# Performance work log

Measured on AMD Instinct MI355X. Metric: run time of the kernel, lower is better.

The kernel has to match this reference:

```python
import jax, jax.numpy as jnp
import numpy as np

U, I, D, L, NNZ, B = 100000, 50000, 64, 3, 3200000, 4096
N = U + I
MOMENTUM = 0.05

def setup_inputs() -> dict:
    key = jax.random.key(0)
    ks = jax.random.split(key, 10)
    return {
        'user_emb': jax.random.normal(ks[0], (U, D), jnp.float32) * 0.02,
        'item_emb': jax.random.normal(ks[1], (I, D), jnp.float32) * 0.02,
        'W': jax.random.normal(ks[2], (D, D), jnp.float32) * (1.0 / np.sqrt(D)),
        'b': jnp.zeros((D,), jnp.float32),
        'adj_rows': jax.random.randint(ks[3], (NNZ,), 0, N, jnp.int32),
        'adj_cols': jax.random.randint(ks[4], (NNZ,), 0, N, jnp.int32),
        'adj_vals': jax.random.uniform(ks[5], (NNZ,), jnp.float32) * 0.05,
        'users': jax.random.randint(ks[6], (B,), 0, U, jnp.int32),
        'items': jax.random.randint(ks[7], (B,), 0, I, jnp.int32),
        'u_his': jax.random.normal(ks[8], (U, D), jnp.float32),
        'i_his': jax.random.normal(ks[9], (I, D), jnp.float32),
    }

def _spmm(rows, cols, vals, x):
    # y = A @ x for sparse COO A: gather source rows, scale, scatter-add to dest rows
    return jax.ops.segment_sum(vals[:, None] * x[cols], rows, num_segments=N)

def reference(user_emb, item_emb, W, b, adj_rows, adj_cols, adj_vals, users, items, u_his, i_his):
    ego = jnp.concatenate([user_emb, item_emb], axis=0)  # [N, D]
    acc = ego
    cur = ego
    for _ in range(L):
        cur = _spmm(adj_rows, adj_cols, adj_vals, cur)
        acc = acc + cur
    all_emb = acc / (L + 1)           # mean over stacked layers
    u_all = all_emb[:U]
    i_all = all_emb[U:]
    u_online = u_all[users]           # [B, D]
    i_online = i_all[items]
    m = MOMENTUM
    u_target = jax.lax.stop_gradient(u_his[users] * m + u_online * (1.0 - m))
    i_target = jax.lax.stop_gradient(i_his[items] * m + i_online * (1.0 - m))
    p_u = u_online @ W.T + b
    p_i = i_online @ W.T + b
    return (p_u, u_target, p_i, i_target)
```

## Files before the change

### kernel.cpp

```cpp
#include <hip/hip_runtime.h>
#include <hip/hip_bf16.h>

#define U_CNT   100000
#define I_CNT   50000
#define D_DIM   64
#define N_NODES 150000
#define NNZ_E   3200000
#define B_SZ    4096

#define NSUB 1172
#define CAP2 4096
#define TILE_E 8192
#define N_TILES ((NNZ_E + TILE_E - 1) / TILE_E)

#define CONV_THREADS (N_NODES * 16)
#define CONV_PER_BLK (512 * 4)
#define CONV_BLOCKS ((CONV_THREADS + CONV_PER_BLK - 1) / CONV_PER_BLK)

typedef unsigned int uint;
typedef unsigned short ushort_t;
typedef _Float16 half_t;
typedef half_t half2_t __attribute__((ext_vector_type(2)));

union h2u_t { uint u; half2_t h; };
__device__ __forceinline__ half2_t u2h2(uint u) { h2u_t c; c.u = u; return c.h; }
__device__ __forceinline__ uint h22u(half2_t h) { h2u_t c; c.h = h; return c.u; }
__device__ __forceinline__ half2_t h2shfl_xor(half2_t v, int m) {
    h2u_t c; c.h = v; c.u = (uint)__shfl_xor((int)c.u, m, 64); return c.h;
}
__device__ __forceinline__ float h2lo(uint u) { return (float)u2h2(u)[0]; }
__device__ __forceinline__ float h2hi(uint u) { return (float)u2h2(u)[1]; }

__global__ __launch_bounds__(512) void scatter_kernel(const int* __restrict__ rows,
                                                      const int* __restrict__ cols,
                                                      const float* __restrict__ vals,
                                                      int* __restrict__ subcursor,
                                                      int2* __restrict__ meta,
                                                      const float4* __restrict__ ue4,
                                                      const float4* __restrict__ ie4,
                                                      uint2* __restrict__ e2) {
    int tid = threadIdx.x;

    if (blockIdx.x >= N_TILES) {
        int g0 = (blockIdx.x - N_TILES) * CONV_PER_BLK + tid;
        #pragma unroll
        for (int k = 0; k < 4; ++k) {
            int g = g0 + k * 512;
            if (g < CONV_THREADS) {
                float4 f = (g < U_CNT * 16) ? ue4[g] : ie4[g - U_CNT * 16];
                half2_t a = { (half_t)f.x, (half_t)f.y };
                half2_t b = { (half_t)f.z, (half_t)f.w };
                uint2 o; o.x = h22u(a); o.y = h22u(b);
                e2[g] = o;
            }
        }
        return;
    }

    __shared__ int lcnt[NSUB];
    __shared__ int gbase[NSUB];

    for (int i = tid; i < NSUB; i += 512) lcnt[i] = 0;
    __syncthreads();

    int base = blockIdx.x * TILE_E;
    int nk = NNZ_E - base - tid;
    nk = (nk <= 0) ? 0 : (nk + 511) >> 9;

    int pk[16]; float vv[16]; int sb[16]; int rk[16];
    #pragma unroll
    for (int k = 0; k < 16; ++k) {
        if (k < nk) {
            int j = base + tid + (k << 9);
            int r = rows[j];
            int c = cols[j];
            vv[k] = vals[j];
            sb[k] = r >> 7;
            pk[k] = ((r & 127) << 18) | c;
            rk[k] = atomicAdd(&lcnt[sb[k]], 1);
        }
    }
    __syncthreads();

    for (int i = tid; i < NSUB; i += 512) {
        int c = lcnt[i];
        int off = (c > 0) ? atomicAdd(&subcursor[i], c) : 0;
        gbase[i] = i * CAP2 + off;
    }
    __syncthreads();

    #pragma unroll
    for (int k = 0; k < 16; ++k) {
        if (k < nk) {
            int pos = gbase[sb[k]] + rk[k];
            if (pos < (sb[k] + 1) * CAP2)
                meta[pos] = make_int2(pk[k], __float_as_int(vv[k]));
        }
    }
}

__global__ __launch_bounds__(512) void sort_spmm_kernel(const int* __restrict__ subcursor,
                                                        int2* __restrict__ meta,
                                                        int* __restrict__ rstart,
                                                        int* __restrict__ rend,
                                                        const ushort_t* __restrict__ x,
                                                        ushort_t* __restrict__ out) {
    __shared__ int2 stage[CAP2];
    __shared__ int rcnt[128];
    __shared__ int rs[128];
    __shared__ int re_[128];
    int g = blockIdx.x;
    int base = g * CAP2;
    int cnt = subcursor[g];
    if (cnt > CAP2) cnt = CAP2;
    int tid = threadIdx.x;
    int r0 = g << 7;

    if (tid < 128) rcnt[tid] = 0;
    __syncthreads();

    int2 ek[8]; int rk[8];
    int nk = cnt - tid;
    nk = (nk <= 0) ? 0 : (nk + 511) >> 9;
    #pragma unroll
    for (int k = 0; k < 8; ++k) {
        if (k < nk) {
            ek[k] = meta[base + tid + (k << 9)];
            rk[k] = atomicAdd(&rcnt[((uint)ek[k].x >> 18) & 127], 1);
        }
    }
    __syncthreads();

    if (tid < 64) {
        int c0 = rcnt[2 * tid], c1 = rcnt[2 * tid + 1];
        int s2 = c0 + c1, incl = s2;
        #pragma unroll
        for (int off = 1; off < 64; off <<= 1) {
            int t = __shfl_up(incl, off, 64);
            if (tid >= off) incl += t;
        }
        int s0 = incl - s2, s1 = incl - c1;
        rs[2 * tid] = s0;      re_[2 * tid] = s0 + c0;
        rs[2 * tid + 1] = s1;  re_[2 * tid + 1] = incl;
        int r = r0 + 2 * tid;
        if (r < N_NODES)     { rstart[r]     = base + s0; rend[r]     = base + s0 + c0; }
        if (r + 1 < N_NODES) { rstart[r + 1] = base + s1; rend[r + 1] = base + incl;    }
    }
    __syncthreads();

    #pragma unroll
    for (int k = 0; k < 8; ++k) {
        if (k < nk) {
            int rl = ((uint)ek[k].x >> 18) & 127;
            int pos = rs[rl] + rk[k];
            float v = __int_as_float(ek[k].y);
            half2_t hv = { (half_t)v, (half_t)v };
            int2 f = make_int2(ek[k].x & 0x3FFFF, (int)h22u(hv));
            stage[pos] = f;
            meta[base + pos] = f;
        }
    }
    __syncthreads();

    int wv   = tid >> 6;
    int lane = tid & 63;
    int sub  = lane >> 3;
    int l8   = lane & 7;
    const uint4* x4 = (const uint4*)x;

    for (int rr = 0; rr < 16; ++rr) {
        int rl = (wv << 4) + rr;
        int s = rs[rl], e = re_[rl];
        half2_t a0 = { (half_t)0, (half_t)0 };
        half2_t a1 = a0, a2 = a0, a3 = a0;

        if (e > s) {
            int last = e - 1;
            auto ldl = [&](int jj) -> int2 {
                int2 c = stage[jj < e ? jj : last];
                if (jj >= e) c.y = 0;
                return c;
            };
            int j = s + sub;
            int2 c0 = ldl(j);
            int2 c1 = ldl(j + 8);
            int2 c2 = ldl(j + 16);
            int2 c3 = ldl(j + 24);
            for (; j < e; j += 32) {
                uint4 x0 = x4[(size_t)(c0.x & 0x3FFFF) * 8 + l8];
                uint4 x1 = x4[(size_t)(c1.x & 0x3FFFF) * 8 + l8];
                uint4 x2 = x4[(size_t)(c2.x & 0x3FFFF) * 8 + l8];
                uint4 x3 = x4[(size_t)(c3.x & 0x3FFFF) * 8 + l8];
                int jn = j + 32;
                int2 n0 = ldl(jn);
                int2 n1 = ldl(jn + 8);
                int2 n2 = ldl(jn + 16);
                int2 n3 = ldl(jn + 24);
                half2_t v0 = u2h2((uint)c0.y);
                a0 += u2h2(x0.x) * v0; a1 += u2h2(x0.y) * v0;
                a2 += u2h2(x0.z) * v0; a3 += u2h2(x0.w) * v0;
                half2_t v1 = u2h2((uint)c1.y);
                a0 += u2h2(x1.x) * v1; a1 += u2h2(x1.y) * v1;
                a2 += u2h2(x1.z) * v1; a3 += u2h2(x1.w) * v1;
                half2_t v2 = u2h2((uint)c2.y);
                a0 += u2h2(x2.x) * v2; a1 += u2h2(x2.y) * v2;
                a2 += u2h2(x2.z) * v2; a3 += u2h2(x2.w) * v2;
                half2_t v3 = u2h2((uint)c3.y);
                a0 += u2h2(x3.x) * v3; a1 += u2h2(x3.y) * v3;
                a2 += u2h2(x3.z) * v3; a3 += u2h2(x3.w) * v3;
                c0 = n0; c1 = n1; c2 = n2; c3 = n3;
            }
        }
        a0 += h2shfl_xor(a0, 8);  a1 += h2shfl_xor(a1, 8);
        a2 += h2shfl_xor(a2, 8);  a3 += h2shfl_xor(a3, 8);
        a0 += h2shfl_xor(a0, 16); a1 += h2shfl_xor(a1, 16);
        a2 += h2shfl_xor(a2, 16); a3 += h2shfl_xor(a3, 16);
        a0 += h2shfl_xor(a0, 32); a1 += h2shfl_xor(a1, 32);
        a2 += h2shfl_xor(a2, 32); a3 += h2shfl_xor(a3, 32);

        int wid = r0 + rl;
        if (sub == 0 && wid < N_NODES) {
            uint4 r;
            r.x = h22u(a0); r.y = h22u(a1); r.z = h22u(a2); r.w = h22u(a3);
            ((uint4*)out)[(size_t)wid * 8 + l8] = r;
        }
    }
}

__global__ __launch_bounds__(256) void spmm_fp16_kernel(const int* __restrict__ rstart,
                                                        const int* __restrict__ rend,
                                                        const int2* __restrict__ csr,
                                                        const ushort_t* __restrict__ x,
                                                        ushort_t* __restrict__ out) {
    int wid  = (blockIdx.x * blockDim.x + threadIdx.x) >> 6;
    int lane = threadIdx.x & 63;
    int sub  = lane >> 3;
    int l8   = lane & 7;
    if (wid >= N_NODES) return;
    int s = rstart[wid], e = rend[wid];
    const uint4* x4 = (const uint4*)x;

    int last = e - 1; if (last < s) last = s;
    auto ld = [&](int jj) -> int2 {
        int2 c = csr[jj < e ? jj : last];
        if (jj >= e) c.y = 0;
        return c;
    };

    half2_t a0 = { (half_t)0, (half_t)0 };
    half2_t a1 = a0, a2 = a0, a3 = a0;

    int j = s + sub;
    int2 c0 = ld(j);
    int2 c1 = ld(j + 8);
    int2 c2 = ld(j + 16);
    int2 c3 = ld(j + 24);
    for (; j < e; j += 32) {
        uint4 x0 = x4[(size_t)(c0.x & 0x3FFFF) * 8 + l8];
        uint4 x1 = x4[(size_t)(c1.x & 0x3FFFF) * 8 + l8];
        uint4 x2 = x4[(size_t)(c2.x & 0x3FFFF) * 8 + l8];
        uint4 x3 = x4[(size_t)(c3.x & 0x3FFFF) * 8 + l8];
        int jn = j + 32;
        int2 n0 = ld(jn);
        int2 n1 = ld(jn + 8);
        int2 n2 = ld(jn + 16);
        int2 n3 = ld(jn + 24);
        half2_t v0 = u2h2((uint)c0.y);
        a0 += u2h2(x0.x) * v0; a1 += u2h2(x0.y) * v0;
        a2 += u2h2(x0.z) * v0; a3 += u2h2(x0.w) * v0;
        half2_t v1 = u2h2((uint)c1.y);
        a0 += u2h2(x1.x) * v1; a1 += u2h2(x1.y) * v1;
        a2 += u2h2(x1.z) * v1; a3 += u2h2(x1.w) * v1;
        half2_t v2 = u2h2((uint)c2.y);
        a0 += u2h2(x2.x) * v2; a1 += u2h2(x2.y) * v2;
        a2 += u2h2(x2.z) * v2; a3 += u2h2(x2.w) * v2;
        half2_t v3 = u2h2((uint)c3.y);
        a0 += u2h2(x3.x) * v3; a1 += u2h2(x3.y) * v3;
        a2 += u2h2(x3.z) * v3; a3 += u2h2(x3.w) * v3;
        c0 = n0; c1 = n1; c2 = n2; c3 = n3;
    }
    a0 += h2shfl_xor(a0, 8);  a1 += h2shfl_xor(a1, 8);
    a2 += h2shfl_xor(a2, 8);  a3 += h2shfl_xor(a3, 8);
    a0 += h2shfl_xor(a0, 16); a1 += h2shfl_xor(a1, 16);
    a2 += h2shfl_xor(a2, 16); a3 += h2shfl_xor(a3, 16);
    a0 += h2shfl_xor(a0, 32); a1 += h2shfl_xor(a1, 32);
    a2 += h2shfl_xor(a2, 32); a3 += h2shfl_xor(a3, 32);

    if (sub == 0) {
        uint4 r;
        r.x = h22u(a0); r.y = h22u(a1); r.z = h22u(a2); r.w = h22u(a3);
        ((uint4*)out)[(size_t)wid * 8 + l8] = r;
    }
}

__global__ __launch_bounds__(256) void epilogue_kernel(const int* __restrict__ users,
                                                       const int* __restrict__ items,
                                                       const int* __restrict__ rstart,
                                                       const int* __restrict__ rend,
                                                       const int2* __restrict__ csr,
                                                       const ushort_t* __restrict__ ebuf,
                                                       const ushort_t* __restrict__ buf1,
                                                       const ushort_t* __restrict__ buf2,
                                                       const float* __restrict__ u_his,
                                                       const float* __restrict__ i_his,
                                                       const float* __restrict__ W,
                                                       const float* __restrict__ bvec,
                                                       float* __restrict__ out) {
    __shared__ float Wt[D_DIM * 65];
    __shared__ float bsh[D_DIM];
    __shared__ float on_s[4][D_DIM];
    for (int t = threadIdx.x; t < D_DIM * D_DIM; t += blockDim.x) {
        int j = t >> 6, k = t & 63;
        Wt[k * 65 + j] = W[t];
    }
    if (threadIdx.x < D_DIM) bsh[threadIdx.x] = bvec[threadIdx.x];

    int wv   = threadIdx.x >> 6;
    int wid  = blockIdx.x * 4 + wv;
    int lane = threadIdx.x & 63;
    int sub  = lane >> 4;
    int l16  = lane & 15;

    bool is_user = (wid < B_SZ);
    int  samp = is_user ? wid : wid - B_SZ;
    int  idx  = is_user ? users[samp] : items[samp];
    int  row  = is_user ? idx : (U_CNT + idx);

    const float* his = is_user ? u_his : i_his;
    float hisv = his[(size_t)idx * D_DIM + lane];
    uint2 eg = make_uint2(0, 0), b1v = eg, b2v = eg;
    if (sub == 0) {
        eg  = ((const uint2*)ebuf)[(size_t)row * 16 + l16];
        b1v = ((const uint2*)buf1)[(size_t)row * 16 + l16];
        b2v = ((const uint2*)buf2)[(size_t)row * 16 + l16];
    }

    int s = rstart[row], e = rend[row];
    int last = e - 1; if (last < s) last = s;
    auto ld = [&](int jj) -> int2 {
        int2 c = csr[jj < e ? jj : last];
        if (jj >= e) c.y = 0;
        return c;
    };
    half2_t c0 = { (half_t)0, (half_t)0 };
    half2_t c1 = c0;
    int j = s + sub;
    int2 e0 = ld(j);
    int2 e1 = ld(j + 4);
    int2 e2 = ld(j + 8);
    int2 e3 = ld(j + 12);
    for (; j < e; j += 16) {
        uint2 x0 = ((const uint2*)buf2)[(size_t)(e0.x & 0x3FFFF) * 16 + l16];
        uint2 x1 = ((const uint2*)buf2)[(size_t)(e1.x & 0x3FFFF) * 16 + l16];
        uint2 x2 = ((const uint2*)buf2)[(size_t)(e2.x & 0x3FFFF) * 16 + l16];
        uint2 x3 = ((const uint2*)buf2)[(size_t)(e3.x & 0x3FFFF) * 16 + l16];
        int jn = j + 16;
        int2 n0 = ld(jn);
        int2 n1 = ld(jn + 4);
        int2 n2 = ld(jn + 8);
        int2 n3 = ld(jn + 12);
        half2_t v0 = u2h2((uint)e0.y);
        c0 += u2h2(x0.x) * v0; c1 += u2h2(x0.y) * v0;
        half2_t v1 = u2h2((uint)e1.y);
        c0 += u2h2(x1.x) * v1; c1 += u2h2(x1.y) * v1;
        half2_t v2 = u2h2((uint)e2.y);
        c0 += u2h2(x2.x) * v2; c1 += u2h2(x2.y) * v2;
        half2_t v3 = u2h2((uint)e3.y);
        c0 += u2h2(x3.x) * v3; c1 += u2h2(x3.y) * v3;
        e0 = n0; e1 = n1; e2 = n2; e3 = n3;
    }
    c0 += h2shfl_xor(c0, 16); c1 += h2shfl_xor(c1, 16);
    c0 += h2shfl_xor(c0, 32); c1 += h2shfl_xor(c1, 32);

    if (sub == 0) {
        on_s[wv][l16 * 4 + 0] = (h2lo(eg.x) + h2lo(b1v.x) + h2lo(b2v.x) + (float)c0[0]) * 0.25f;
        on_s[wv][l16 * 4 + 1] = (h2hi(eg.x) + h2hi(b1v.x) + h2hi(b2v.x) + (float)c0[1]) * 0.25f;
        on_s[wv][l16 * 4 + 2] = (h2lo(eg.y) + h2lo(b1v.y) + h2lo(b2v.y) + (float)c1[0]) * 0.25f;
        on_s[wv][l16 * 4 + 3] = (h2hi(eg.y) + h2hi(b1v.y) + h2hi(b2v.y) + (float)c1[1]) * 0.25f;
    }
    __syncthreads();

    float online = on_s[wv][lane];
    float target = 0.05f * hisv + 0.95f * online;

    float p = bsh[lane];
    #pragma unroll
    for (int k = 0; k < D_DIM; ++k) {
        float ok = __shfl(online, k, 64);
        p = fmaf(ok, Wt[k * 65 + lane], p);
    }

    size_t base = is_user ? 0 : (size_t)2 * B_SZ * D_DIM;
    out[base + (size_t)samp * D_DIM + lane] = p;
    out[base + (size_t)B_SZ * D_DIM + (size_t)samp * D_DIM + lane] = target;
}


extern "C" void kernel_launch(void* const* d_in, const int* in_sizes, int n_in,
                              void* d_out, int out_size, void* d_ws, size_t ws_size,
                              hipStream_t stream) {
    const float* user_emb = (const float*)d_in[0];
    const float* item_emb = (const float*)d_in[1];
    const float* W        = (const float*)d_in[2];
    const float* bvec     = (const float*)d_in[3];
    const int*   adj_rows = (const int*)d_in[4];
    const int*   adj_cols = (const int*)d_in[5];
    const float* adj_vals = (const float*)d_in[6];
    const int*   users    = (const int*)d_in[7];
    const int*   items    = (const int*)d_in[8];
    const float* u_his    = (const float*)d_in[9];
    const float* i_his    = (const float*)d_in[10];
    float* out = (float*)d_out;

    char* ws = (char*)d_ws;
    size_t o = 0;
    ushort_t* ebuf  = (ushort_t*)(ws + o); o += (size_t)N_NODES * D_DIM * 2;
    ushort_t* buf1  = (ushort_t*)(ws + o); o += (size_t)N_NODES * D_DIM * 2;
    ushort_t* buf2  = (ushort_t*)(ws + o); o += (size_t)N_NODES * D_DIM * 2;
    int2*  meta     = (int2*)(ws + o);     o += (size_t)NSUB * CAP2 * 8;
    int*   rstart   = (int*)(ws + o);      o += (size_t)N_NODES * 4;
    int*   rend     = (int*)(ws + o);      o += (size_t)N_NODES * 4;
    int*   subcursor= (int*)(ws + o);      o += (size_t)NSUB * 4;
    (void)ws_size; (void)o; (void)in_sizes; (void)n_in; (void)out_size;

    hipMemsetAsync(subcursor, 0, (size_t)NSUB * 4, stream);

    scatter_kernel<<<N_TILES + CONV_BLOCKS, 512, 0, stream>>>(
        adj_rows, adj_cols, adj_vals, subcursor, meta,
        (const float4*)user_emb, (const float4*)item_emb, (uint2*)ebuf);

    sort_spmm_kernel<<<NSUB, 512, 0, stream>>>(subcursor, meta, rstart, rend,
                                               ebuf, buf1);

    int spmm_blocks = (N_NODES + 3) / 4;
    spmm_fp16_kernel<<<spmm_blocks, 256, 0, stream>>>(rstart, rend, meta, buf1, buf2);

    epilogue_kernel<<<(2 * B_SZ) / 4, 256, 0, stream>>>(users, items, rstart, rend, meta,
                                                        ebuf, buf1, buf2,
                                                        u_his, i_his, W, bvec, out);
}
```

Measured before the change: 329.0 us.

## Partition scatter cursors eightfold and process two rows per wave in SpMM

```diff
diff --git a/kernel.cpp b/kernel.cpp
--- a/kernel.cpp
+++ b/kernel.cpp
@@ -10,6 +10,8 @@
 
 #define NSUB 1172
 #define CAP2 4096
+#define NPART 8
+#define CAPP 512
 #define TILE_E 8192
 #define N_TILES ((NNZ_E + TILE_E - 1) / TILE_E)
 
@@ -34,8 +36,8 @@
 __global__ __launch_bounds__(512) void scatter_kernel(const int* __restrict__ rows,
                                                       const int* __restrict__ cols,
                                                       const float* __restrict__ vals,
-                                                      int* __restrict__ subcursor,
-                                                      int2* __restrict__ meta,
+                                                      int* __restrict__ pcursor,
+                                                      int2* __restrict__ pmeta,
                                                       const float4* __restrict__ ue4,
                                                       const float4* __restrict__ ie4,
                                                       uint2* __restrict__ e2) {
@@ -58,7 +60,8 @@
     }
 
     __shared__ int lcnt[NSUB];
-    __shared__ int gbase[NSUB];
+    __shared__ int gofs[NSUB];
+    int part = blockIdx.x & (NPART - 1);
 
     for (int i = tid; i < NSUB; i += 512) lcnt[i] = 0;
     __syncthreads();
@@ -84,23 +87,24 @@
 
     for (int i = tid; i < NSUB; i += 512) {
         int c = lcnt[i];
-        int off = (c > 0) ? atomicAdd(&subcursor[i], c) : 0;
-        gbase[i] = i * CAP2 + off;
+        gofs[i] = (c > 0) ? atomicAdd(&pcursor[part * NSUB + i], c) : 0;
     }
     __syncthreads();
 
     #pragma unroll
     for (int k = 0; k < 16; ++k) {
         if (k < nk) {
-            int pos = gbase[sb[k]] + rk[k];
-            if (pos < (sb[k] + 1) * CAP2)
-                meta[pos] = make_int2(pk[k], __float_as_int(vv[k]));
-        }
-    }
-}
-
-__global__ __launch_bounds__(512) void sort_spmm_kernel(const int* __restrict__ subcursor,
-                                                        int2* __restrict__ meta,
+            int cellpos = gofs[sb[k]] + rk[k];
+            if (cellpos < CAPP)
+                pmeta[((size_t)(part * NSUB + sb[k])) * CAPP + cellpos] =
+                    make_int2(pk[k], __float_as_int(vv[k]));
+        }
+    }
+}
+
+__global__ __launch_bounds__(512) void sort_spmm_kernel(const int* __restrict__ pcursor,
+                                                        const int2* __restrict__ pmeta,
+                                                        int2* __restrict__ meta2,
                                                         int* __restrict__ rstart,
                                                         int* __restrict__ rend,
                                                         const ushort_t* __restrict__ x,
@@ -109,24 +113,31 @@
     __shared__ int rcnt[128];
     __shared__ int rs[128];
     __shared__ int re_[128];
+    __shared__ int cur[128];
     int g = blockIdx.x;
     int base = g * CAP2;
-    int cnt = subcursor[g];
-    if (cnt > CAP2) cnt = CAP2;
     int tid = threadIdx.x;
     int r0 = g << 7;
 
+    int cnt_p[NPART], pfx[NPART];
+    int cnt = 0;
+    #pragma unroll
+    for (int p = 0; p < NPART; ++p) {
+        int c = pcursor[p * NSUB + g];
+        if (c > CAPP) c = CAPP;
+        cnt_p[p] = c; pfx[p] = cnt; cnt += c;
+    }
+
     if (tid < 128) rcnt[tid] = 0;
     __syncthreads();
 
-    int2 ek[8]; int rk[8];
-    int nk = cnt - tid;
-    nk = (nk <= 0) ? 0 : (nk + 511) >> 9;
     #pragma unroll
-    for (int k = 0; k < 8; ++k) {
-        if (k < nk) {
-            ek[k] = meta[base + tid + (k << 9)];
-            rk[k] = atomicAdd(&rcnt[((uint)ek[k].x >> 18) & 127], 1);
+    for (int p = 0; p < NPART; ++p) {
+        const int2* seg = &pmeta[((size_t)(p * NSUB + g)) * CAPP];
+        for (int i = tid; i < cnt_p[p]; i += 512) {
+            int2 e = seg[i];
+            stage[pfx[p] + i] = e;
+            atomicAdd(&rcnt[((uint)e.x >> 18) & 127], 1);
         }
     }
     __syncthreads();
@@ -140,26 +151,25 @@
             if (tid >= off) incl += t;
         }
         int s0 = incl - s2, s1 = incl - c1;
-        rs[2 * tid] = s0;      re_[2 * tid] = s0 + c0;
-        rs[2 * tid + 1] = s1;  re_[2 * tid + 1] = incl;
+        rs[2 * tid] = s0;      re_[2 * tid] = s0 + c0;     cur[2 * tid] = s0;
+        rs[2 * tid + 1] = s1;  re_[2 * tid + 1] = incl;    cur[2 * tid + 1] = s1;
         int r = r0 + 2 * tid;
         if (r < N_NODES)     { rstart[r]     = base + s0; rend[r]     = base + s0 + c0; }
         if (r + 1 < N_NODES) { rstart[r + 1] = base + s1; rend[r + 1] = base + incl;    }
     }
     __syncthreads();
 
-    #pragma unroll
-    for (int k = 0; k < 8; ++k) {
-        if (k < nk) {
-            int rl = ((uint)ek[k].x >> 18) & 127;
-            int pos = rs[rl] + rk[k];
-            float v = __int_as_float(ek[k].y);
-            half2_t hv = { (half_t)v, (half_t)v };
-            int2 f = make_int2(ek[k].x & 0x3FFFF, (int)h22u(hv));
-            stage[pos] = f;
-            meta[base + pos] = f;
-        }
-    }
+    for (int i = tid; i < cnt; i += 512) {
+        int2 e = stage[i];
+        int rl = ((uint)e.x >> 18) & 127;
+        int pos = atomicAdd(&cur[rl], 1);
+        float v = __int_as_float(e.y);
+        half2_t hv = { (half_t)v, (half_t)v };
+        meta2[base + pos] = make_int2(e.x & 0x3FFFF, (int)h22u(hv));
+    }
+    __syncthreads();
+
+    for (int i = tid; i < cnt; i += 512) stage[i] = meta2[base + i];
     __syncthreads();
 
     int wv   = tid >> 6;
@@ -232,64 +242,103 @@
                                                         const int2* __restrict__ csr,
                                                         const ushort_t* __restrict__ x,
                                                         ushort_t* __restrict__ out) {
-    int wid  = (blockIdx.x * blockDim.x + threadIdx.x) >> 6;
+    int gw   = (blockIdx.x * blockDim.x + threadIdx.x) >> 6;
     int lane = threadIdx.x & 63;
     int sub  = lane >> 3;
     int l8   = lane & 7;
-    if (wid >= N_NODES) return;
-    int s = rstart[wid], e = rend[wid];
+    int wid0 = gw * 2, wid1 = gw * 2 + 1;
+    if (wid0 >= N_NODES) return;
     const uint4* x4 = (const uint4*)x;
 
-    int last = e - 1; if (last < s) last = s;
-    auto ld = [&](int jj) -> int2 {
-        int2 c = csr[jj < e ? jj : last];
-        if (jj >= e) c.y = 0;
+    int s0 = rstart[wid0], e0 = rend[wid0];
+    int s1 = 0, e1 = 0;
+    if (wid1 < N_NODES) { s1 = rstart[wid1]; e1 = rend[wid1]; }
+    int last0 = (e0 - 1 < s0) ? s0 : e0 - 1;
+    int last1 = (e1 - 1 < s1) ? s1 : e1 - 1;
+
+    auto ld0 = [&](int jj) -> int2 {
+        int2 c = csr[jj < e0 ? jj : last0];
+        if (jj >= e0) c.y = 0;
         return c;
     };
-
-    half2_t a0 = { (half_t)0, (half_t)0 };
-    half2_t a1 = a0, a2 = a0, a3 = a0;
-
-    int j = s + sub;
-    int2 c0 = ld(j);
-    int2 c1 = ld(j + 8);
-    int2 c2 = ld(j + 16);
-    int2 c3 = ld(j + 24);
-    for (; j < e; j += 32) {
-        uint4 x0 = x4[(size_t)(c0.x & 0x3FFFF) * 8 + l8];
-        uint4 x1 = x4[(size_t)(c1.x & 0x3FFFF) * 8 + l8];
-        uint4 x2 = x4[(size_t)(c2.x & 0x3FFFF) * 8 + l8];
-        uint4 x3 = x4[(size_t)(c3.x & 0x3FFFF) * 8 + l8];
-        int jn = j + 32;
-        int2 n0 = ld(jn);
-        int2 n1 = ld(jn + 8);
-        int2 n2 = ld(jn + 16);
-        int2 n3 = ld(jn + 24);
-        half2_t v0 = u2h2((uint)c0.y);
-        a0 += u2h2(x0.x) * v0; a1 += u2h2(x0.y) * v0;
-        a2 += u2h2(x0.z) * v0; a3 += u2h2(x0.w) * v0;
-        half2_t v1 = u2h2((uint)c1.y);
-        a0 += u2h2(x1.x) * v1; a1 += u2h2(x1.y) * v1;
-        a2 += u2h2(x1.z) * v1; a3 += u2h2(x1.w) * v1;
-        half2_t v2 = u2h2((uint)c2.y);
-        a0 += u2h2(x2.x) * v2; a1 += u2h2(x2.y) * v2;
-        a2 += u2h2(x2.z) * v2; a3 += u2h2(x2.w) * v2;
-        half2_t v3 = u2h2((uint)c3.y);
-        a0 += u2h2(x3.x) * v3; a1 += u2h2(x3.y) * v3;
-        a2 += u2h2(x3.z) * v3; a3 += u2h2(x3.w) * v3;
-        c0 = n0; c1 = n1; c2 = n2; c3 = n3;
-    }
-    a0 += h2shfl_xor(a0, 8);  a1 += h2shfl_xor(a1, 8);
-    a2 += h2shfl_xor(a2, 8);  a3 += h2shfl_xor(a3, 8);
-    a0 += h2shfl_xor(a0, 16); a1 += h2shfl_xor(a1, 16);
-    a2 += h2shfl_xor(a2, 16); a3 += h2shfl_xor(a3, 16);
-    a0 += h2shfl_xor(a0, 32); a1 += h2shfl_xor(a1, 32);
-    a2 += h2shfl_xor(a2, 32); a3 += h2shfl_xor(a3, 32);
+    auto ld1 = [&](int jj) -> int2 {
+        int2 c = csr[jj < e1 ? jj : last1];
+        if (jj >= e1) c.y = 0;
+        return c;
+    };
+
+    half2_t z = { (half_t)0, (half_t)0 };
+    half2_t a00 = z, a01 = z, a02 = z, a03 = z;
+    half2_t a10 = z, a11 = z, a12 = z, a13 = z;
+
+    int j0 = s0 + sub, j1 = s1 + sub;
+    int2 c00 = ld0(j0), c01 = ld0(j0 + 8), c02 = ld0(j0 + 16), c03 = ld0(j0 + 24);
+    int2 c10 = ld1(j1), c11 = ld1(j1 + 8), c12 = ld1(j1 + 16), c13 = ld1(j1 + 24);
+    while (j0 < e0 || j1 < e1) {
+        uint4 x00 = x4[(size_t)(c00.x & 0x3FFFF) * 8 + l8];
+        uint4 x01 = x4[(size_t)(c01.x & 0x3FFFF) * 8 + l8];
+        uint4 x02 = x4[(size_t)(c02.x & 0x3FFFF) * 8 + l8];
+        uint4 x03 = x4[(size_t)(c03.x & 0x3FFFF) * 8 + l8];
+        uint4 x10 = x4[(size_t)(c10.x & 0x3FFFF) * 8 + l8];
+        uint4 x11 = x4[(size_t)(c11.x & 0x3FFFF) * 8 + l8];
+        uint4 x12 = x4[(size_t)(c12.x & 0x3FFFF) * 8 + l8];
+        uint4 x13 = x4[(size_t)(c13.x & 0x3FFFF) * 8 + l8];
+        int jn0 = j0 + 32, jn1 = j1 + 32;
+        int2 n00 = ld0(jn0), n01 = ld0(jn0 + 8), n02 = ld0(jn0 + 16), n03 = ld0(jn0 + 24);
+        int2 n10 = ld1(jn1), n11 = ld1(jn1 + 8), n12 = ld1(jn1 + 16), n13 = ld1(jn1 + 24);
+
+        half2_t v;
+        v = u2h2((uint)c00.y);
+        a00 += u2h2(x00.x) * v; a01 += u2h2(x00.y) * v;
+        a02 += u2h2(x00.z) * v; a03 += u2h2(x00.w) * v;
+        v = u2h2((uint)c10.y);
+        a10 += u2h2(x10.x) * v; a11 += u2h2(x10.y) * v;
+        a12 += u2h2(x10.z) * v; a13 += u2h2(x10.w) * v;
+        v = u2h2((uint)c01.y);
+        a00 += u2h2(x01.x) * v; a01 += u2h2(x01.y) * v;
+        a02 += u2h2(x01.z) * v; a03 += u2h2(x01.w) * v;
+        v = u2h2((uint)c11.y);
+        a10 += u2h2(x11.x) * v; a11 += u2h2(x11.y) * v;
+        a12 += u2h2(x11.z) * v; a13 += u2h2(x11.w) * v;
+        v = u2h2((uint)c02.y);
+        a00 += u2h2(x02.x) * v; a01 += u2h2(x02.y) * v;
+        a02 += u2h2(x02.z) * v; a03 += u2h2(x02.w) * v;
+        v = u2h2((uint)c12.y);
+        a10 += u2h2(x12.x) * v; a11 += u2h2(x12.y) * v;
+        a12 += u2h2(x12.z) * v; a13 += u2h2(x12.w) * v;
+        v = u2h2((uint)c03.y);
+        a00 += u2h2(x03.x) * v; a01 += u2h2(x03.y) * v;
+        a02 += u2h2(x03.z) * v; a03 += u2h2(x03.w) * v;
+        v = u2h2((uint)c13.y);
+        a10 += u2h2(x13.x) * v; a11 += u2h2(x13.y) * v;
+        a12 += u2h2(x13.z) * v; a13 += u2h2(x13.w) * v;
+
+        c00 = n00; c01 = n01; c02 = n02; c03 = n03;
+        c10 = n10; c11 = n11; c12 = n12; c13 = n13;
+        j0 = jn0; j1 = jn1;
+    }
+    a00 += h2shfl_xor(a00, 8);  a01 += h2shfl_xor(a01, 8);
+    a02 += h2shfl_xor(a02, 8);  a03 += h2shfl_xor(a03, 8);
+    a10 += h2shfl_xor(a10, 8);  a11 += h2shfl_xor(a11, 8);
+    a12 += h2shfl_xor(a12, 8);  a13 += h2shfl_xor(a13, 8);
+    a00 += h2shfl_xor(a00, 16); a01 += h2shfl_xor(a01, 16);
+    a02 += h2shfl_xor(a02, 16); a03 += h2shfl_xor(a03, 16);
+    a10 += h2shfl_xor(a10, 16); a11 += h2shfl_xor(a11, 16);
+    a12 += h2shfl_xor(a12, 16); a13 += h2shfl_xor(a13, 16);
+    a00 += h2shfl_xor(a00, 32); a01 += h2shfl_xor(a01, 32);
+    a02 += h2shfl_xor(a02, 32); a03 += h2shfl_xor(a03, 32);
+    a10 += h2shfl_xor(a10, 32); a11 += h2shfl_xor(a11, 32);
+    a12 += h2shfl_xor(a12, 32); a13 += h2shfl_xor(a13, 32);
 
     if (sub == 0) {
         uint4 r;
-        r.x = h22u(a0); r.y = h22u(a1); r.z = h22u(a2); r.w = h22u(a3);
-        ((uint4*)out)[(size_t)wid * 8 + l8] = r;
+        r.x = h22u(a00); r.y = h22u(a01); r.z = h22u(a02); r.w = h22u(a03);
+        ((uint4*)out)[(size_t)wid0 * 8 + l8] = r;
+    }
+    if (sub == 1 && wid1 < N_NODES) {
+        uint4 r;
+        r.x = h22u(a10); r.y = h22u(a11); r.z = h22u(a12); r.w = h22u(a13);
+        ((uint4*)out)[(size_t)wid1 * 8 + l8] = r;
     }
 }
 
@@ -417,25 +466,26 @@
     ushort_t* ebuf  = (ushort_t*)(ws + o); o += (size_t)N_NODES * D_DIM * 2;
     ushort_t* buf1  = (ushort_t*)(ws + o); o += (size_t)N_NODES * D_DIM * 2;
     ushort_t* buf2  = (ushort_t*)(ws + o); o += (size_t)N_NODES * D_DIM * 2;
-    int2*  meta     = (int2*)(ws + o);     o += (size_t)NSUB * CAP2 * 8;
+    int2*  pmeta    = (int2*)(ws + o);     o += (size_t)NPART * NSUB * CAPP * 8;
+    int2*  meta2    = (int2*)(ws + o);     o += (size_t)NSUB * CAP2 * 8;
     int*   rstart   = (int*)(ws + o);      o += (size_t)N_NODES * 4;
     int*   rend     = (int*)(ws + o);      o += (size_t)N_NODES * 4;
-    int*   subcursor= (int*)(ws + o);      o += (size_t)NSUB * 4;
+    int*   pcursor  = (int*)(ws + o);      o += (size_t)NPART * NSUB * 4;
     (void)ws_size; (void)o; (void)in_sizes; (void)n_in; (void)out_size;
 
-    hipMemsetAsync(subcursor, 0, (size_t)NSUB * 4, stream);
+    hipMemsetAsync(pcursor, 0, (size_t)NPART * NSUB * 4, stream);
 
     scatter_kernel<<<N_TILES + CONV_BLOCKS, 512, 0, stream>>>(
-        adj_rows, adj_cols, adj_vals, subcursor, meta,
+        adj_rows, adj_cols, adj_vals, pcursor, pmeta,
         (const float4*)user_emb, (const float4*)item_emb, (uint2*)ebuf);
 
-    sort_spmm_kernel<<<NSUB, 512, 0, stream>>>(subcursor, meta, rstart, rend,
+    sort_spmm_kernel<<<NSUB, 512, 0, stream>>>(pcursor, pmeta, meta2, rstart, rend,
                                                ebuf, buf1);
 
-    int spmm_blocks = (N_NODES + 3) / 4;
-    spmm_fp16_kernel<<<spmm_blocks, 256, 0, stream>>>(rstart, rend, meta, buf1, buf2);
-
-    epilogue_kernel<<<(2 * B_SZ) / 4, 256, 0, stream>>>(users, items, rstart, rend, meta,
+    int spmm_blocks = ((N_NODES + 1) / 2 + 3) / 4;
+    spmm_fp16_kernel<<<spmm_blocks, 256, 0, stream>>>(rstart, rend, meta2, buf1, buf2);
+
+    epilogue_kernel<<<(2 * B_SZ) / 4, 256, 0, stream>>>(users, items, rstart, rend, meta2,
                                                         ebuf, buf1, buf2,
                                                         u_his, i_his, W, bvec, out);
 }
```

Result: faster. 317.6 us (-3.5%).
